# Performance work log

Measured on AMD Instinct MI355X. Metric: run time of the kernel, lower is better.

The kernel has to match this reference:

```python
import jax, jax.numpy as jnp
import numpy as np

B, N, M = 4, 2048, 2048
DIM = 1024
HEADS = 16
DIM_HEAD = 64
INNER = HEADS * DIM_HEAD
SCALE = 8.0


def layer_norm(x, g, eps=1e-5):
    mean = jnp.mean(x, axis=-1, keepdims=True)
    var = jnp.mean((x - mean) ** 2, axis=-1, keepdims=True)
    return (x - mean) * jax.lax.rsqrt(var + eps) * g


def l2norm(t, eps=1e-12):
    n = jnp.maximum(jnp.linalg.norm(t, axis=-1, keepdims=True), eps)
    return t / n


def setup_inputs() -> dict:
    key = jax.random.key(0)
    ks = jax.random.split(key, 8)
    x = jax.random.normal(ks[0], (B, N, DIM), dtype=jnp.float32)
    context = jax.random.normal(ks[1], (B, M, DIM), dtype=jnp.float32)
    # parameters
    g_norm = jnp.ones((DIM,), dtype=jnp.float32)
    null_kv = jax.random.normal(ks[2], (2, DIM_HEAD), dtype=jnp.float32)
    Wq = jax.random.normal(ks[3], (DIM, INNER), dtype=jnp.float32) / np.sqrt(DIM)
    Wkv = jax.random.normal(ks[4], (DIM, 2 * INNER), dtype=jnp.float32) / np.sqrt(DIM)
    q_scale = jnp.ones((DIM_HEAD,), dtype=jnp.float32)
    k_scale = jnp.ones((DIM_HEAD,), dtype=jnp.float32)
    Wout = jax.random.normal(ks[5], (INNER, DIM), dtype=jnp.float32) / np.sqrt(INNER)
    g_out = jnp.ones((DIM,), dtype=jnp.float32)
    return {"x": x, "context": context, "g_norm": g_norm, "null_kv": null_kv,
            "Wq": Wq, "Wkv": Wkv, "q_scale": q_scale, "k_scale": k_scale,
            "Wout": Wout, "g_out": g_out}


def reference(x, context, g_norm, null_kv, Wq, Wkv, q_scale, k_scale, Wout, g_out):
    b = x.shape[0]
    xn = layer_norm(x, g_norm)            # [b, n, dim]
    ctx = context                          # norm_context=False -> Identity
    q = xn @ Wq                            # [b, n, inner]
    kv = ctx @ Wkv                         # [b, m, 2*inner]
    k, v = jnp.split(kv, 2, axis=-1)
    split_heads = lambda t: t.reshape(b, t.shape[1], HEADS, DIM_HEAD).transpose(0, 2, 1, 3)
    q, k, v = map(split_heads, (q, k, v))  # [b, h, n|m, d]
    # null kv token prepended along the key/value sequence dim
    nk = jnp.broadcast_to(null_kv[0], (b, HEADS, 1, DIM_HEAD))
    nv = jnp.broadcast_to(null_kv[1], (b, HEADS, 1, DIM_HEAD))
    k = jnp.concatenate([nk, k], axis=2)   # [b, h, m+1, d]
    v = jnp.concatenate([nv, v], axis=2)
    # QK-norm with learned per-dim scales
    q = l2norm(q) * q_scale
    k = l2norm(k) * k_scale
    sim = jnp.einsum('bhid,bhjd->bhij', q, k) * SCALE
    attn = jax.nn.softmax(sim.astype(jnp.float32), axis=-1).astype(sim.dtype)
    out = jnp.einsum('bhij,bhjd->bhid', attn, v)
    out = out.transpose(0, 2, 1, 3).reshape(b, -1, INNER)  # [b, n, inner]
    out = out @ Wout
    return layer_norm(out, g_out)
```

## Files before the change

kernel.cpp:

```cpp
#include <hip/hip_runtime.h>

#define BATCH 4
#define NSEQ 2048
#define MSEQ 2048
#define DIM 1024
#define HEADS 16
#define DHEAD 64
#define INNER 1024
#define KVLEN 2049
#define KVPAD 2176

typedef unsigned short u16;
typedef unsigned int u32;
typedef __bf16 bf16x8 __attribute__((ext_vector_type(8)));
typedef float f32x4 __attribute__((ext_vector_type(4)));

__device__ inline u16 f2bf(float f) {
  u32 u = __builtin_bit_cast(u32, f);
  u = (u + 0x7fffu + ((u >> 16) & 1u)) >> 16;
  return (u16)u;
}
__device__ inline float bf2f(u16 x) {
  return __builtin_bit_cast(float, (u32)x << 16);
}
__device__ inline u32 pk_bf16(float lo, float hi) {
  u32 r;
  asm("v_cvt_pk_bf16_f32 %0, %1, %2" : "=v"(r) : "v"(lo), "v"(hi));
  return r;
}

__device__ __forceinline__ void gld_lds16(const void* g, void* l) {
  __builtin_amdgcn_global_load_lds(
      (const __attribute__((address_space(1))) void*)g,
      (__attribute__((address_space(3))) void*)l, 16, 0, 0);
}

template <bool OUT_BF16>
__global__ __launch_bounds__(256) void ln_kernel(const float* __restrict__ x,
                                                 const float* __restrict__ g,
                                                 void* __restrict__ out) {
  const int row = blockIdx.x;
  const int t = threadIdx.x;
  const float4 v = ((const float4*)(x + (size_t)row * 1024))[t];
  float sum = v.x + v.y + v.z + v.w;
  float sq = v.x * v.x + v.y * v.y + v.z * v.z + v.w * v.w;
  for (int m = 1; m < 64; m <<= 1) {
    sum += __shfl_xor(sum, m, 64);
    sq += __shfl_xor(sq, m, 64);
  }
  __shared__ float red[8];
  const int w = t >> 6, l = t & 63;
  if (l == 0) { red[w] = sum; red[4 + w] = sq; }
  __syncthreads();
  sum = red[0] + red[1] + red[2] + red[3];
  sq = red[4] + red[5] + red[6] + red[7];
  const float mean = sum * (1.0f / 1024.0f);
  const float var = sq * (1.0f / 1024.0f) - mean * mean;
  const float rstd = rsqrtf(var + 1e-5f);
  const float4 gv = ((const float4*)g)[t];
  float o0 = (v.x - mean) * rstd * gv.x;
  float o1 = (v.y - mean) * rstd * gv.y;
  float o2 = (v.z - mean) * rstd * gv.z;
  float o3 = (v.w - mean) * rstd * gv.w;
  if (OUT_BF16) {
    ushort4 ov;
    ov.x = f2bf(o0); ov.y = f2bf(o1); ov.z = f2bf(o2); ov.w = f2bf(o3);
    ((ushort4*)((u16*)out + (size_t)row * 1024))[t] = ov;
  } else {
    float4 ov;
    ov.x = o0; ov.y = o1; ov.z = o2; ov.w = o3;
    ((float4*)((float*)out + (size_t)row * 1024))[t] = ov;
  }
}

__global__ __launch_bounds__(256) void cast_bf16(const float* __restrict__ in,
                                                 u16* __restrict__ out, int n4) {
  int i = blockIdx.x * 256 + threadIdx.x;
  if (i < n4) {
    float4 v = ((const float4*)in)[i];
    ushort4 o;
    o.x = f2bf(v.x); o.y = f2bf(v.y); o.z = f2bf(v.z); o.w = f2bf(v.w);
    ((ushort4*)out)[i] = o;
  }
}

__global__ __launch_bounds__(256) void transpose_cast(const float* __restrict__ W,
                                                      u16* __restrict__ WT, int K, int N) {
  __shared__ float tile[32][33];
  const int tx = threadIdx.x & 31, ty = threadIdx.x >> 5;
  const int k0 = blockIdx.y * 32, n0 = blockIdx.x * 32;
  for (int r = ty; r < 32; r += 8) tile[r][tx] = W[(size_t)(k0 + r) * N + n0 + tx];
  __syncthreads();
  for (int r = ty; r < 32; r += 8) WT[(size_t)(n0 + r) * K + k0 + tx] = f2bf(tile[tx][r]);
}

template <int MODE>
__global__ __launch_bounds__(256) void gemm_bt(const u16* __restrict__ A,
                                               const u16* __restrict__ Bt,
                                               void* __restrict__ Cv,
                                               int M, int N, int K,
                                               const float* __restrict__ scale,
                                               u16* __restrict__ aux) {
  __shared__ __align__(16) u16 As[128 * 32];
  __shared__ __align__(16) u16 Bs[128 * 32];
  const int t = threadIdx.x;
  const int w = t >> 6, l = t & 63, l15 = l & 15, lq = l >> 4;
  const int m0 = blockIdx.y * 128, n0 = blockIdx.x * 128;
  const int wm = (w >> 1) * 64, wn = (w & 1) * 64;
  const int lr = l >> 2;
  const int lo = (l & 3) * 8;
  f32x4 acc[4][4] = {};
  for (int k0 = 0; k0 < K; k0 += 32) {
#pragma unroll
    for (int it = 0; it < 2; it++) {
      const int row = (w * 2 + it) * 16 + lr;
      gld_lds16(&A[(size_t)(m0 + row) * K + k0 + lo], &As[row * 32 + lo]);
      gld_lds16(&Bt[(size_t)(n0 + row) * K + k0 + lo], &Bs[row * 32 + lo]);
    }
    __syncthreads();
    bf16x8 af[4], bfr[4];
#pragma unroll
    for (int i = 0; i < 4; i++) af[i] = *(bf16x8*)&As[(wm + i * 16 + l15) * 32 + lq * 8];
#pragma unroll
    for (int j = 0; j < 4; j++) bfr[j] = *(bf16x8*)&Bs[(wn + j * 16 + l15) * 32 + lq * 8];
#pragma unroll
    for (int i = 0; i < 4; i++)
#pragma unroll
      for (int j = 0; j < 4; j++)
        acc[i][j] = __builtin_amdgcn_mfma_f32_16x16x32_bf16(af[i], bfr[j], acc[i][j], 0, 0, 0);
    __syncthreads();
  }

  if (MODE <= 1) {
#pragma unroll
    for (int i = 0; i < 4; i++)
#pragma unroll
      for (int j = 0; j < 4; j++)
#pragma unroll
        for (int r = 0; r < 4; r++) {
          const size_t off =
              (size_t)(m0 + wm + i * 16 + lq * 4 + r) * N + n0 + wn + j * 16 + l15;
          if (MODE == 1) ((u16*)Cv)[off] = f2bf(acc[i][j][r]);
          else ((float*)Cv)[off] = acc[i][j][r];
        }
    return;
  }

  const int head = (n0 + wn) >> 6;
  if (MODE == 3 && head >= 16) {
#pragma unroll
    for (int i = 0; i < 4; i++)
#pragma unroll
      for (int j = 0; j < 4; j++)
#pragma unroll
        for (int r = 0; r < 4; r++) {
          const int row = m0 + wm + i * 16 + lq * 4 + r;
          aux[(size_t)row * 1024 + (head - 16) * 64 + j * 16 + l15] = f2bf(acc[i][j][r]);
        }
    return;
  }
  float sc[4];
#pragma unroll
  for (int j = 0; j < 4; j++) sc[j] = scale[j * 16 + l15];
  const float mul = (MODE == 2) ? 8.0f : 1.0f;
  u16* outp = (u16*)Cv;
#pragma unroll
  for (int i = 0; i < 4; i++)
#pragma unroll
    for (int r = 0; r < 4; r++) {
      float ss = 0.f;
#pragma unroll
      for (int j = 0; j < 4; j++) ss = fmaf(acc[i][j][r], acc[i][j][r], ss);
#pragma unroll
      for (int m = 1; m < 16; m <<= 1) ss += __shfl_xor(ss, m, 64);
      const float inv = mul / fmaxf(sqrtf(ss), 1e-12f);
      const int row = m0 + wm + i * 16 + lq * 4 + r;
      const int b = row >> 11, n = row & 2047;
      const size_t base = (MODE == 2)
          ? (((size_t)b * 16 + head) * 2048 + n) * 64
          : (((size_t)b * 16 + head) * (size_t)KVPAD + n + 1) * 64;
#pragma unroll
      for (int j = 0; j < 4; j++)
        outp[base + j * 16 + l15] = f2bf(acc[i][j][r] * inv * sc[j]);
    }
}

__global__ __launch_bounds__(256) void v_post(const u16* __restrict__ vg,
                                              u16* __restrict__ vt) {
  __shared__ u16 tile[64][68];
  const int bh = blockIdx.y, mt = blockIdx.x;
  const int tx = threadIdx.x & 63, ty = threadIdx.x >> 6;
  const int b = bh >> 4, h = bh & 15;
  const int m0 = mt * 64;
  for (int r = ty; r < 64; r += 4)
    tile[tx][r] = vg[(size_t)(b * 2048 + m0 + r) * 1024 + h * 64 + tx];
  __syncthreads();
  const int abs_ = 1 + m0 + tx;
  const int a = abs_ & 127;
  const int slot = (abs_ & ~127) | (a & 0x63) | ((a & 0x10) >> 2) | ((a & 0x0C) << 1);
  for (int d = ty; d < 64; d += 4)
    vt[((size_t)bh * 64 + d) * KVPAD + slot] = tile[d][tx];
}

__global__ __launch_bounds__(256) void null_tail(const float* __restrict__ null_kv,
                                                 const float* __restrict__ k_scale,
                                                 u16* __restrict__ kn, u16* __restrict__ vt) {
  const int bh = blockIdx.x, t = threadIdx.x;
  const int d = t & 63, seg = t >> 6;
  if (seg == 0) {
    float nk = null_kv[d];
    float nv = null_kv[64 + d];
    float ss = nk * nk;
    for (int m = 1; m < 64; m <<= 1) ss += __shfl_xor(ss, m, 64);
    float inv = 1.0f / fmaxf(sqrtf(ss), 1e-12f);
    kn[((size_t)bh * KVPAD) * 64 + d] = f2bf(nk * inv * k_scale[d]);
    vt[((size_t)bh * 64 + d) * KVPAD] = f2bf(nv);
  }
  for (int m = KVLEN + seg; m < KVPAD; m += 4) kn[((size_t)bh * KVPAD + m) * 64 + d] = 0;
  u16* vrow = vt + ((size_t)bh * 64 + d) * KVPAD;
  for (int m = KVLEN + seg; m < KVPAD; m += 4) vrow[m] = 0;
}

__global__ __launch_bounds__(256, 6) void attn_kernel(const u16* __restrict__ qn,
                                                      const u16* __restrict__ kn,
                                                      const u16* __restrict__ vt,
                                                      u16* __restrict__ aout) {
  __shared__ __align__(16) u16 Ks[64 * 64];
  __shared__ __align__(16) u16 Vs[64 * 64];
  const int qt = blockIdx.x, bh = blockIdx.y;
  const int b = bh >> 4, h = bh & 15;
  const int t = threadIdx.x, w = t >> 6, l = t & 63, l15 = l & 15, lq = l >> 4;

  bf16x8 aqf[2];
  {
    const u16* qrow = qn + ((size_t)bh * 2048 + qt * 64 + w * 16 + l15) * 64 + lq * 8;
    aqf[0] = *(const bf16x8*)(qrow);
    aqf[1] = *(const bf16x8*)(qrow + 32);
  }

  const uint4 onesu = {0x3F803F80u, 0x3F803F80u, 0x3F803F80u, 0x3F803F80u};
  const bf16x8 vones = __builtin_bit_cast(bf16x8, onesu);

  int so[2];
#pragma unroll
  for (int i = 0; i < 2; i++) so[i] = ((i * 4 + lq) ^ (l15 & 7)) * 8;

  const u16* kn_b = kn + (size_t)bh * KVPAD * 64;
  const u16* vt_b = vt + (size_t)bh * 64 * KVPAD;
  const u16* ksrc[2];
  const u16* vsrc[2];
#pragma unroll
  for (int i = 0; i < 2; i++) {
    const int row = i * 32 + w * 8 + (l >> 3);
    const int sl = (l & 7) ^ (l >> 3);
    ksrc[i] = kn_b + row * 64 + sl * 8;
    vsrc[i] = vt_b + (size_t)row * KVPAD + sl * 8;
  }
  u16* kdst = &Ks[w * 512 + l * 8];
  u16* vdst = &Vs[w * 512 + l * 8];

  f32x4 O[4] = {};
  f32x4 lsacc = {};
  const float LOG2E = 1.44269504f;
  const float MBIAS = -8.0f * 1.44269504f;

  for (int kt = 0; kt < 33; kt++) {
#pragma unroll
    for (int i = 0; i < 2; i++) {
      gld_lds16(ksrc[i] + kt * 4096, kdst + i * 2048);
      gld_lds16(vsrc[i] + kt * 64, vdst + i * 2048);
    }
    __syncthreads();

    f32x4 St[4] = {};
    __builtin_amdgcn_s_setprio(1);
#pragma unroll
    for (int ks = 0; ks < 2; ks++)
#pragma unroll
      for (int j = 0; j < 4; j++) {
        bf16x8 ak = *(bf16x8*)&Ks[(j * 16 + l15) * 64 + so[ks]];
        St[j] = __builtin_amdgcn_mfma_f32_16x16x32_bf16(ak, aqf[ks], St[j], 0, 0, 0);
      }
    __builtin_amdgcn_s_setprio(0);

    float p[4][4];
#pragma unroll
    for (int j = 0; j < 4; j++)
#pragma unroll
      for (int r = 0; r < 4; r++)
        p[j][r] = __builtin_amdgcn_exp2f(fmaf(St[j][r], LOG2E, MBIAS));
    if (kt == 32) {
#pragma unroll
      for (int j = 0; j < 4; j++)
#pragma unroll
        for (int r = 0; r < 4; r++)
          if ((j | r) != 0) p[j][r] = 0.f;
      if (lq != 0) p[0][0] = 0.f;
    }
    bf16x8 pa[2];
#pragma unroll
    for (int m = 0; m < 2; m++) {
      uint4 pw;
      pw.x = pk_bf16(p[2 * m][0], p[2 * m][1]);
      pw.y = pk_bf16(p[2 * m][2], p[2 * m][3]);
      pw.z = pk_bf16(p[2 * m + 1][0], p[2 * m + 1][1]);
      pw.w = pk_bf16(p[2 * m + 1][2], p[2 * m + 1][3]);
      pa[m] = __builtin_bit_cast(bf16x8, pw);
    }

    __builtin_amdgcn_s_setprio(1);
#pragma unroll
    for (int m = 0; m < 2; m++) {
      lsacc = __builtin_amdgcn_mfma_f32_16x16x32_bf16(pa[m], vones, lsacc, 0, 0, 0);
#pragma unroll
      for (int nt = 0; nt < 4; nt++) {
        bf16x8 bv = *(bf16x8*)&Vs[(nt * 16 + l15) * 64 + so[m]];
        O[nt] = __builtin_amdgcn_mfma_f32_16x16x32_bf16(pa[m], bv, O[nt], 0, 0, 0);
      }
    }
    __builtin_amdgcn_s_setprio(0);
    __syncthreads();
  }

  float inv[4];
#pragma unroll
  for (int r = 0; r < 4; r++) inv[r] = 1.0f / lsacc[r];
#pragma unroll
  for (int nt = 0; nt < 4; nt++)
#pragma unroll
    for (int r = 0; r < 4; r++) {
      int row = qt * 64 + w * 16 + lq * 4 + r;
      int col = h * 64 + nt * 16 + l15;
      float val = O[nt][r] * inv[r];
      aout[((size_t)b * 2048 + row) * 1024 + col] = f2bf(val);
    }
}

extern "C" void kernel_launch(void* const* d_in, const int* in_sizes, int n_in,
                              void* d_out, int out_size, void* d_ws, size_t ws_size,
                              hipStream_t stream) {
  const float* x = (const float*)d_in[0];
  const float* context = (const float*)d_in[1];
  const float* g_norm = (const float*)d_in[2];
  const float* null_kv = (const float*)d_in[3];
  const float* Wq = (const float*)d_in[4];
  const float* Wkv = (const float*)d_in[5];
  const float* q_scale = (const float*)d_in[6];
  const float* k_scale = (const float*)d_in[7];
  const float* Wout = (const float*)d_in[8];
  const float* g_out = (const float*)d_in[9];
  float* out = (float*)d_out;

  char* ws = (char*)d_ws;
  u16* xn = (u16*)(ws);
  u16* ctxb = (u16*)(ws + 16777216);
  u16* wqT = (u16*)(ws + 33554432);
  u16* wkvT = (u16*)(ws + 35651584);
  u16* woutT = (u16*)(ws + 39845888);
  u16* qnb = (u16*)(ws + 41943040);
  u16* knb = (u16*)(ws + 58720256);
  u16* vtb = (u16*)(ws + 76546048);
  u16* vg = (u16*)(ws + 94371840);
  float* outg = (float*)(ws + 111149056);
  u16* attn_out = vg;

  ln_kernel<true><<<8192, 256, 0, stream>>>(x, g_norm, xn);
  cast_bf16<<<8192, 256, 0, stream>>>(context, ctxb, 2097152);
  transpose_cast<<<dim3(32, 32), 256, 0, stream>>>(Wq, wqT, 1024, 1024);
  transpose_cast<<<dim3(64, 32), 256, 0, stream>>>(Wkv, wkvT, 1024, 2048);
  transpose_cast<<<dim3(32, 32), 256, 0, stream>>>(Wout, woutT, 1024, 1024);
  gemm_bt<2><<<dim3(8, 64), 256, 0, stream>>>(xn, wqT, qnb, 8192, 1024, 1024, q_scale, nullptr);
  gemm_bt<3><<<dim3(16, 64), 256, 0, stream>>>(ctxb, wkvT, knb, 8192, 2048, 1024, k_scale, vg);
  v_post<<<dim3(32, 64), 256, 0, stream>>>(vg, vtb);
  null_tail<<<64, 256, 0, stream>>>(null_kv, k_scale, knb, vtb);
  attn_kernel<<<dim3(32, 64), 256, 0, stream>>>(qnb, knb, vtb, attn_out);
  gemm_bt<0><<<dim3(8, 64), 256, 0, stream>>>(attn_out, woutT, outg, 8192, 1024, 1024, nullptr, nullptr);
  ln_kernel<false><<<8192, 256, 0, stream>>>(outg, g_out, out);
}
```

Before: 414.6 us.

## Process two 16-row query tiles per wave to reuse K/V LDS loads

Each attention block now covers 128 query rows instead of 64, with every wave holding two Q fragments and two sets of S, O and row-sum accumulators. Each K and V tile staged in LDS, and each fragment read from it, is reused for twice as many MFMAs, halving global K/V traffic and LDS reads per query. In exchange, register use roughly doubles, launch bounds drop from 6 to 4 waves per SIMD, and the grid halves to 1024 blocks, which reduces parallelism and latency hiding.

```diff
diff --git a/kernel.cpp b/kernel.cpp
--- a/kernel.cpp
+++ b/kernel.cpp
@@ -221,7 +221,7 @@
   for (int m = KVLEN + seg; m < KVPAD; m += 4) vrow[m] = 0;
 }
 
-__global__ __launch_bounds__(256, 6) void attn_kernel(const u16* __restrict__ qn,
+__global__ __launch_bounds__(256, 4) void attn_kernel(const u16* __restrict__ qn,
                                                       const u16* __restrict__ kn,
                                                       const u16* __restrict__ vt,
                                                       u16* __restrict__ aout) {
@@ -231,11 +231,13 @@
   const int b = bh >> 4, h = bh & 15;
   const int t = threadIdx.x, w = t >> 6, l = t & 63, l15 = l & 15, lq = l >> 4;
 
-  bf16x8 aqf[2];
-  {
-    const u16* qrow = qn + ((size_t)bh * 2048 + qt * 64 + w * 16 + l15) * 64 + lq * 8;
-    aqf[0] = *(const bf16x8*)(qrow);
-    aqf[1] = *(const bf16x8*)(qrow + 32);
+  bf16x8 aqf[2][2];
+#pragma unroll
+  for (int i = 0; i < 2; i++) {
+    const u16* qrow =
+        qn + ((size_t)bh * 2048 + qt * 128 + w * 32 + i * 16 + l15) * 64 + lq * 8;
+    aqf[i][0] = *(const bf16x8*)(qrow);
+    aqf[i][1] = *(const bf16x8*)(qrow + 32);
   }
 
   const uint4 onesu = {0x3F803F80u, 0x3F803F80u, 0x3F803F80u, 0x3F803F80u};
@@ -259,8 +261,8 @@
   u16* kdst = &Ks[w * 512 + l * 8];
   u16* vdst = &Vs[w * 512 + l * 8];
 
-  f32x4 O[4] = {};
-  f32x4 lsacc = {};
+  f32x4 O[2][4] = {};
+  f32x4 lsacc[2] = {};
   const float LOG2E = 1.44269504f;
   const float MBIAS = -8.0f * 1.44269504f;
 
@@ -272,68 +274,81 @@
     }
     __syncthreads();
 
-    f32x4 St[4] = {};
+    f32x4 St[2][4] = {};
     __builtin_amdgcn_s_setprio(1);
 #pragma unroll
     for (int ks = 0; ks < 2; ks++)
 #pragma unroll
       for (int j = 0; j < 4; j++) {
         bf16x8 ak = *(bf16x8*)&Ks[(j * 16 + l15) * 64 + so[ks]];
-        St[j] = __builtin_amdgcn_mfma_f32_16x16x32_bf16(ak, aqf[ks], St[j], 0, 0, 0);
+        St[0][j] = __builtin_amdgcn_mfma_f32_16x16x32_bf16(ak, aqf[0][ks], St[0][j], 0, 0, 0);
+        St[1][j] = __builtin_amdgcn_mfma_f32_16x16x32_bf16(ak, aqf[1][ks], St[1][j], 0, 0, 0);
       }
     __builtin_amdgcn_s_setprio(0);
 
-    float p[4][4];
-#pragma unroll
-    for (int j = 0; j < 4; j++)
-#pragma unroll
-      for (int r = 0; r < 4; r++)
-        p[j][r] = __builtin_amdgcn_exp2f(fmaf(St[j][r], LOG2E, MBIAS));
+    float p[2][4][4];
+#pragma unroll
+    for (int i = 0; i < 2; i++)
+#pragma unroll
+      for (int j = 0; j < 4; j++)
+#pragma unroll
+        for (int r = 0; r < 4; r++)
+          p[i][j][r] = __builtin_amdgcn_exp2f(fmaf(St[i][j][r], LOG2E, MBIAS));
     if (kt == 32) {
 #pragma unroll
-      for (int j = 0; j < 4; j++)
-#pragma unroll
-        for (int r = 0; r < 4; r++)
-          if ((j | r) != 0) p[j][r] = 0.f;
-      if (lq != 0) p[0][0] = 0.f;
-    }
-    bf16x8 pa[2];
+      for (int i = 0; i < 2; i++) {
+#pragma unroll
+        for (int j = 0; j < 4; j++)
+#pragma unroll
+          for (int r = 0; r < 4; r++)
+            if ((j | r) != 0) p[i][j][r] = 0.f;
+        if (lq != 0) p[i][0][0] = 0.f;
+      }
+    }
+    bf16x8 pa[2][2];
+#pragma unroll
+    for (int i = 0; i < 2; i++)
+#pragma unroll
+      for (int m = 0; m < 2; m++) {
+        uint4 pw;
+        pw.x = pk_bf16(p[i][2 * m][0], p[i][2 * m][1]);
+        pw.y = pk_bf16(p[i][2 * m][2], p[i][2 * m][3]);
+        pw.z = pk_bf16(p[i][2 * m + 1][0], p[i][2 * m + 1][1]);
+        pw.w = pk_bf16(p[i][2 * m + 1][2], p[i][2 * m + 1][3]);
+        pa[i][m] = __builtin_bit_cast(bf16x8, pw);
+      }
+
+    __builtin_amdgcn_s_setprio(1);
 #pragma unroll
     for (int m = 0; m < 2; m++) {
-      uint4 pw;
-      pw.x = pk_bf16(p[2 * m][0], p[2 * m][1]);
-      pw.y = pk_bf16(p[2 * m][2], p[2 * m][3]);
-      pw.z = pk_bf16(p[2 * m + 1][0], p[2 * m + 1][1]);
-      pw.w = pk_bf16(p[2 * m + 1][2], p[2 * m + 1][3]);
-      pa[m] = __builtin_bit_cast(bf16x8, pw);
-    }
-
-    __builtin_amdgcn_s_setprio(1);
-#pragma unroll
-    for (int m = 0; m < 2; m++) {
-      lsacc = __builtin_amdgcn_mfma_f32_16x16x32_bf16(pa[m], vones, lsacc, 0, 0, 0);
+      lsacc[0] = __builtin_amdgcn_mfma_f32_16x16x32_bf16(pa[0][m], vones, lsacc[0], 0, 0, 0);
+      lsacc[1] = __builtin_amdgcn_mfma_f32_16x16x32_bf16(pa[1][m], vones, lsacc[1], 0, 0, 0);
 #pragma unroll
       for (int nt = 0; nt < 4; nt++) {
         bf16x8 bv = *(bf16x8*)&Vs[(nt * 16 + l15) * 64 + so[m]];
-        O[nt] = __builtin_amdgcn_mfma_f32_16x16x32_bf16(pa[m], bv, O[nt], 0, 0, 0);
+        O[0][nt] = __builtin_amdgcn_mfma_f32_16x16x32_bf16(pa[0][m], bv, O[0][nt], 0, 0, 0);
+        O[1][nt] = __builtin_amdgcn_mfma_f32_16x16x32_bf16(pa[1][m], bv, O[1][nt], 0, 0, 0);
       }
     }
     __builtin_amdgcn_s_setprio(0);
     __syncthreads();
   }
 
-  float inv[4];
-#pragma unroll
-  for (int r = 0; r < 4; r++) inv[r] = 1.0f / lsacc[r];
-#pragma unroll
-  for (int nt = 0; nt < 4; nt++)
-#pragma unroll
-    for (int r = 0; r < 4; r++) {
-      int row = qt * 64 + w * 16 + lq * 4 + r;
-      int col = h * 64 + nt * 16 + l15;
-      float val = O[nt][r] * inv[r];
-      aout[((size_t)b * 2048 + row) * 1024 + col] = f2bf(val);
-    }
+#pragma unroll
+  for (int i = 0; i < 2; i++) {
+    float inv[4];
+#pragma unroll
+    for (int r = 0; r < 4; r++) inv[r] = 1.0f / lsacc[i][r];
+#pragma unroll
+    for (int nt = 0; nt < 4; nt++)
+#pragma unroll
+      for (int r = 0; r < 4; r++) {
+        int row = qt * 128 + w * 32 + i * 16 + lq * 4 + r;
+        int col = h * 64 + nt * 16 + l15;
+        float val = O[i][nt][r] * inv[r];
+        aout[((size_t)b * 2048 + row) * 1024 + col] = f2bf(val);
+      }
+  }
 }
 
 extern "C" void kernel_launch(void* const* d_in, const int* in_sizes, int n_in,
@@ -373,7 +388,7 @@
   gemm_bt<3><<<dim3(16, 64), 256, 0, stream>>>(ctxb, wkvT, knb, 8192, 2048, 1024, k_scale, vg);
   v_post<<<dim3(32, 64), 256, 0, stream>>>(vg, vtb);
   null_tail<<<64, 256, 0, stream>>>(null_kv, k_scale, knb, vtb);
-  attn_kernel<<<dim3(32, 64), 256, 0, stream>>>(qnb, knb, vtb, attn_out);
+  attn_kernel<<<dim3(16, 64), 256, 0, stream>>>(qnb, knb, vtb, attn_out);
   gemm_bt<0><<<dim3(8, 64), 256, 0, stream>>>(attn_out, woutT, outg, 8192, 1024, 1024, nullptr, nullptr);
   ln_kernel<false><<<8192, 256, 0, stream>>>(outg, g_out, out);
 }
```

New measurement: 395.0 us. -4.7%, faster.
